# Kernel optimization log

Hardware: AMD Instinct MI355X
Metric: run time of the kernel (lower is better)

## Reference

```python
import jax, jax.numpy as jnp
import numpy as np

H = 8  # num_heads
NEG = -1000000.0

def _ln(x, g, b):
    m = jnp.mean(x, axis=-1, keepdims=True)
    v = jnp.var(x, axis=-1, keepdims=True)
    return (x - m) / jnp.sqrt(v + 1e-5) * g + b


def setup_inputs() -> dict:
    key = jax.random.key(0)
    ks = jax.random.split(key, 24)
    B, T, D = 8, 1024, 1024
    Lt, Nt, K, Rt, E = 768, 77, 2, 512, 2048
    s = 0.02
    r = lambda i, shape: s * jax.random.normal(ks[i], shape, jnp.float32)
    return {
        "x": jax.random.normal(ks[0], (B, T, D), jnp.float32),
        "xf": jax.random.normal(ks[1], (B, Nt, Lt), jnp.float32),
        "emb": jax.random.normal(ks[2], (B, E), jnp.float32),
        "src_mask": jnp.ones((B, T, 1), jnp.float32),
        "cond_type": jax.random.randint(ks[3], (B, 1, 1), 0, 100),
        "re_motion": jax.random.normal(ks[4], (B, K, Rt, D), jnp.float32),
        "re_text": jax.random.normal(ks[5], (B, K, 1, D), jnp.float32),
        "re_mask": jnp.ones((B, K, Rt), jnp.float32),
        "ln_g": jnp.ones((D,)), "ln_b": jnp.zeros((D,)),
        "tln_g": jnp.ones((Lt,)), "tln_b": jnp.zeros((Lt,)),
        "rn1_g": jnp.ones((2 * D,)), "rn1_b": jnp.zeros((2 * D,)),
        "rn2_g": jnp.ones((D,)), "rn2_b": jnp.zeros((D,)),
        "Wq": r(6, (D, D)), "bq": jnp.zeros((D,)),
        "Wkt": r(7, (Lt, D)), "bkt": jnp.zeros((D,)),
        "Wvt": r(8, (Lt, D)), "bvt": jnp.zeros((D,)),
        "Wkm": r(9, (D, D)), "bkm": jnp.zeros((D,)),
        "Wvm": r(10, (D, D)), "bvm": jnp.zeros((D,)),
        "Wkr": r(11, (2 * D, D)), "bkr": jnp.zeros((D,)),
        "Wvr": r(12, (D, D)), "bvr": jnp.zeros((D,)),  # zero-init in original; random here for nontrivial math
        "We": r(13, (E, 2 * D)), "be": jnp.zeros((2 * D,)),
        "sln_g": jnp.ones((D,)), "sln_b": jnp.zeros((D,)),
        "Wo": r(14, (D, D)), "bo": jnp.zeros((D,)),  # zero-init in original
    }


def reference(x, xf, emb, src_mask, cond_type, re_motion, re_text, re_mask,
              ln_g, ln_b, tln_g, tln_b, rn1_g, rn1_b, rn2_g, rn2_b,
              Wq, bq, Wkt, bkt, Wvt, bvt, Wkm, bkm, Wvm, bvm,
              Wkr, bkr, Wvr, bvr, We, be, sln_g, sln_b, Wo, bo):
    B, T, D = x.shape
    K, Rt = re_motion.shape[1], re_motion.shape[2]

    norm_x = _ln(x, ln_g, ln_b)
    norm_xf = _ln(xf, tln_g, tln_b)
    query = norm_x @ Wq + bq  # (B,T,D)

    text_ct = (cond_type % 10 > 0).astype(x.dtype)   # (B,1,1)
    retr_ct = (cond_type // 10 > 0).astype(x.dtype)  # (B,1,1)
    re_mask_r = re_mask.reshape(B, -1, 1)            # (B,K*Rt,1)

    # retrieval key features: concat(motion, repeated text) along channels
    re_text_rep = jnp.broadcast_to(re_text, (B, K, Rt, D))
    re_feat_key = jnp.concatenate([re_motion, re_text_rep], axis=-1).reshape(B, -1, 2 * D)

    key_text = norm_xf @ Wkt + bkt + (1.0 - text_ct) * NEG
    key_retr = _ln(re_feat_key, rn1_g, rn1_b) @ Wkr + bkr \
        + (1.0 - retr_ct) * NEG + (1.0 - re_mask_r) * NEG
    key_motion = norm_x @ Wkm + bkm + (1.0 - src_mask) * NEG
    key = jnp.concatenate([key_text, key_retr, key_motion], axis=1)  # (B,N,D)
    N = key.shape[1]

    q = jax.nn.softmax(query.reshape(B, T, H, -1), axis=-1)  # softmax over head dim
    k = jax.nn.softmax(key.reshape(B, N, H, -1), axis=1)     # softmax over tokens

    value_text = (norm_xf @ Wvt + bvt) * text_ct
    value_retr = (_ln(re_motion.reshape(B, -1, D), rn2_g, rn2_b) @ Wvr + bvr) * retr_ct * re_mask_r
    value_motion = (norm_x @ Wvm + bvm) * src_mask
    v = jnp.concatenate([value_text, value_retr, value_motion], axis=1).reshape(B, N, H, -1)

    att = jnp.einsum('bnhd,bnhl->bhdl', k, v)          # (B,H,dh,dh)
    y = jnp.einsum('bthd,bhdl->bthl', q, att).reshape(B, T, D)

    # StylizationBlock: FiLM from time embedding, then zero-init out proj (eval: dropout = id)
    eo = jax.nn.silu(emb) @ We + be                    # (B,2D)
    scale, shift = jnp.split(eo[:, None, :], 2, axis=2)
    h = _ln(y, sln_g, sln_b) * (1.0 + scale) + shift
    h = jax.nn.silu(h) @ Wo + bo
    return x + h
```

## Files before the change

### kernel.cpp

```cpp
#include <hip/hip_runtime.h>
#include <hip/hip_bf16.h>
#include <math.h>

using bf16 = __hip_bfloat16;

typedef short s16x8 __attribute__((ext_vector_type(8)));
typedef short s16x4 __attribute__((ext_vector_type(4)));
typedef float f32x4 __attribute__((ext_vector_type(4)));

constexpr int Bc = 8, Tc = 1024, Dc = 1024, Hc = 8;
constexpr int NTc = 77, LTc = 768, KRc = 1024, Nc = 2125, Ec = 2048;
constexpr float NEGC = -1000000.0f;

constexpr int NP = 2128;
constexpr long SKT = (long)Dc * NP;

constexpr long F_STATS1 = 0;
constexpr long F_STATS2 = F_STATS1 + 16384;
constexpr long F_KEYADD = F_STATS2 + 16384;
constexpr long F_VALMUL = F_KEYADD + 17000;
constexpr long F_SILU   = F_VALMUL + 17000;
constexpr long F_EO     = F_SILU + 16384;
constexpr long F_ATT    = F_EO + 16384;
constexpr long F_END    = F_ATT + 1048576;
// ... 158 lines not shown
__global__ __launch_bounds__(256) void transpose_all(
    const float* __restrict__ Wq,  const float* __restrict__ Wkt,
    const float* __restrict__ Wvt, const float* __restrict__ Wkm,
    const float* __restrict__ Wvm, const float* __restrict__ Wkr,
    const float* __restrict__ Wvr, const float* __restrict__ Wo,
    short* __restrict__ WtQ,  short* __restrict__ WtKT,
    short* __restrict__ WtVT, short* __restrict__ WtKM,
    short* __restrict__ WtVM, short* __restrict__ WtKR,
    short* __restrict__ WtVR, short* __restrict__ WtO) {
    __shared__ float t[32][33];
    int sy = blockIdx.y;
    const float* W; short* Wt; int K; int ky;
    if (sy < 32)       { W = Wq;  Wt = WtQ;  K = 1024; ky = sy; }
    else if (sy < 56)  { W = Wkt; Wt = WtKT; K = 768;  ky = sy - 32; }
    else if (sy < 80)  { W = Wvt; Wt = WtVT; K = 768;  ky = sy - 56; }
    else if (sy < 112) { W = Wkm; Wt = WtKM; K = 1024; ky = sy - 80; }
    else if (sy < 144) { W = Wvm; Wt = WtVM; K = 1024; ky = sy - 112; }
    else if (sy < 208) { W = Wkr; Wt = WtKR; K = 2048; ky = sy - 144; }
    else if (sy < 240) { W = Wvr; Wt = WtVR; K = 1024; ky = sy - 208; }
    else               { W = Wo;  Wt = WtO;  K = 1024; ky = sy - 240; }
    int n0 = blockIdx.x * 32, k0 = ky * 32;
    int tx = threadIdx.x & 31, ty = threadIdx.x >> 5;
    #pragma unroll
    for (int i = 0; i < 4; ++i)
        t[ty + i * 8][tx] = W[(long)(k0 + ty + i * 8) * 1024 + n0 + tx];
    __syncthreads();
    #pragma unroll
    for (int i = 0; i < 4; ++i)
        Wt[(long)(n0 + ty + i * 8) * K + k0 + tx] = f2s(t[tx][ty + i * 8]);
}

constexpr int LDK = 64;

template <typename TC, bool TR = false>
__global__ __launch_bounds__(256) void gemm_bt(
    const short* __restrict__ A, int lda, long sA,
    const short* __restrict__ Bt, int ldb,
    const float* __restrict__ bias,
    const float* __restrict__ rowadd, int sRA,
    const float* __restrict__ rowmul, int sRM,
    const float* __restrict__ addC, int ldac, long sAC,
    TC* __restrict__ C, int ldc, long sC,
    int M, int K) {
    int bz = blockIdx.z;
    A += (long)bz * sA;
    C += (long)bz * sC;
    if (rowadd) rowadd += (long)bz * sRA;
    if (rowmul) rowmul += (long)bz * sRM;
    if (addC) addC += (long)bz * sAC;

    const int tm = blockIdx.y * 128;
    const int tn = blockIdx.x * 128;

    __shared__ __align__(16) short As[128 * LDK];
    __shared__ __align__(16) short Bs[128 * LDK];

    int tid = threadIdx.x;
    int lane = tid & 63, wid = tid >> 6;
    int wi = wid >> 1, wj = wid & 1;
    int l16 = lane & 15, quad = lane >> 4;

    f32x4 acc[4][4];
    #pragma unroll
    for (int i = 0; i < 4; ++i)
        #pragma unroll
        for (int j = 0; j < 4; ++j)
            acc[i][j] = (f32x4){0.f, 0.f, 0.f, 0.f};

    auto issue = [&](int k0) {
        #pragma unroll
        for (int p = 0; p < 4; ++p) {
            int e = p * 256 + tid;
            int row = e >> 3, c8 = e & 7;
            int gm = tm + row;
            if (gm >= M) gm = M - 1;
            gl_lds16(A + (long)gm * lda + k0 + c8 * 8, &As[row * LDK + c8 * 8]);
            gl_lds16(Bt + (long)(tn + row) * ldb + k0 + c8 * 8, &Bs[row * LDK + c8 * 8]);
        }
    };

    issue(0);
    int kt = 0;
    while (true) {
        __syncthreads();
        #pragma unroll
        for (int kk = 0; kk < 2; ++kk) {
            s16x8 af[4], bfr[4];
            #pragma unroll
            for (int i = 0; i < 4; ++i)
                af[i] = *(const s16x8*)&As[(wi * 64 + i * 16 + l16) * LDK + kk * 32 + quad * 8];
            #pragma unroll
            for (int j = 0; j < 4; ++j)
                bfr[j] = *(const s16x8*)&Bs[(wj * 64 + j * 16 + l16) * LDK + kk * 32 + quad * 8];
            #pragma unroll
            for (int i = 0; i < 4; ++i)
                #pragma unroll
                for (int j = 0; j < 4; ++j) {
                    if constexpr (TR)
                        acc[i][j] = __builtin_amdgcn_mfma_f32_16x16x32_bf16(bfr[j], af[i], acc[i][j], 0, 0, 0);
                    else
                        acc[i][j] = __builtin_amdgcn_mfma_f32_16x16x32_bf16(af[i], bfr[j], acc[i][j], 0, 0, 0);
                }
        }
        int nxt = kt + 64;
        if (nxt >= K) break;
        __syncthreads();
        issue(nxt);
        kt = nxt;
    }

    if constexpr (TR) {
        #pragma unroll
        for (int j = 0; j < 4; ++j) {
            #pragma unroll
            for (int r = 0; r < 4; ++r) {
                int feat = tn + wj * 64 + j * 16 + quad * 4 + r;
                float bf_ = bias ? bias[feat] : 0.f;
                #pragma unroll
                for (int i = 0; i < 4; ++i) {
                    int tok = tm + wi * 64 + i * 16 + l16;
                    if (tok >= M) continue;
                    float v = acc[i][j][r] + bf_ + (rowadd ? rowadd[tok] : 0.f);
                    v *= (rowmul ? rowmul[tok] : 1.f);
                    storef(&C[(long)feat * ldc + tok], v);
                }
            }
        }
    } else {
        #pragma unroll
        for (int i = 0; i < 4; ++i) {
            #pragma unroll
            for (int r = 0; r < 4; ++r) {
                int gm = tm + wi * 64 + i * 16 + quad * 4 + r;
                if (gm >= M) continue;
                float ra = rowadd ? rowadd[gm] : 0.f;
                float rm = rowmul ? rowmul[gm] : 1.f;
                #pragma unroll
                for (int j = 0; j < 4; ++j) {
                    int gn = tn + wj * 64 + j * 16 + l16;
                    float v = acc[i][j][r] + (bias ? bias[gn] : 0.f) + ra;
                    v *= rm;
                    if (addC) v += addC[(long)gm * ldac + gn];
                    storef(&C[(long)gm * ldc + gn], v);
                }
            }
        }
    }
}

__global__ __launch_bounds__(256) void gemm_qkvm(
    const short* __restrict__ A, const short* __restrict__ Bt,
    const float* __restrict__ bq, const float* __restrict__ bkm,
    const float* __restrict__ bvm,
    const float* __restrict__ key_add, const float* __restrict__ val_mul,
    bf16* __restrict__ q16, bf16* __restrict__ kT, bf16* __restrict__ vT) {
    const int tm = blockIdx.y * 128;
    const int tn = blockIdx.x * 128;
    const int sec = tn >> 10;
    const int fn0 = tn & 1023;

    __shared__ __align__(16) short As[128 * LDK];
    __shared__ __align__(16) short Bs[128 * LDK];

    int tid = threadIdx.x;
    int lane = tid & 63, wid = tid >> 6;
    int wi = wid >> 1, wj = wid & 1;
    int l16 = lane & 15, quad = lane >> 4;

    f32x4 acc[4][4];
    #pragma unroll
    for (int i = 0; i < 4; ++i)
        #pragma unroll
        for (int j = 0; j < 4; ++j)
            acc[i][j] = (f32x4){0.f, 0.f, 0.f, 0.f};

    auto issue = [&](int k0) {
        #pragma unroll
        for (int p = 0; p < 4; ++p) {
            int e = p * 256 + tid;
            int row = e >> 3, c8 = e & 7;
            gl_lds16(A + (long)(tm + row) * 1024 + k0 + c8 * 8, &As[row * LDK + c8 * 8]);
            gl_lds16(Bt + (long)(tn + row) * 1024 + k0 + c8 * 8, &Bs[row * LDK + c8 * 8]);
        }
    };

    issue(0);
    int kt = 0;
    while (true) {
        __syncthreads();
        #pragma unroll
        for (int kk = 0; kk < 2; ++kk) {
            s16x8 af[4], bfr[4];
            #pragma unroll
            for (int i = 0; i < 4; ++i)
                af[i] = *(const s16x8*)&As[(wi * 64 + i * 16 + l16) * LDK + kk * 32 + quad * 8];
            #pragma unroll
            for (int j = 0; j < 4; ++j)
                bfr[j] = *(const s16x8*)&Bs[(wj * 64 + j * 16 + l16) * LDK + kk * 32 + quad * 8];
            if (sec == 0) {
                #pragma unroll
                for (int i = 0; i < 4; ++i)
                    #pragma unroll
                    for (int j = 0; j < 4; ++j)
                        acc[i][j] = __builtin_amdgcn_mfma_f32_16x16x32_bf16(af[i], bfr[j], acc[i][j], 0, 0, 0);
            } else {
                #pragma unroll
                for (int i = 0; i < 4; ++i)
                    #pragma unroll
                    for (int j = 0; j < 4; ++j)
                        acc[i][j] = __builtin_amdgcn_mfma_f32_16x16x32_bf16(bfr[j], af[i], acc[i][j], 0, 0, 0);
            }
        }
        int nxt = kt + 64;
        if (nxt >= 1024) break;
        __syncthreads();
        issue(nxt);
        kt = nxt;
    }

    if (sec == 0) {
        #pragma unroll
        for (int i = 0; i < 4; ++i) {
            #pragma unroll
            for (int r = 0; r < 4; ++r) {
                int gm = tm + wi * 64 + i * 16 + quad * 4 + r;
                #pragma unroll
                for (int j = 0; j < 4; ++j) {
                    int gn = fn0 + wj * 64 + j * 16 + l16;
                    q16[(long)gm * Dc + gn] = f2b(acc[i][j][r] + bq[gn]);
                }
            }
        }
    } else {
        const float* bias = (sec == 1) ? bkm : bvm;
        bf16* C = (sec == 1) ? kT : vT;
        #pragma unroll
        for (int j = 0; j < 4; ++j) {
            #pragma unroll
            for (int r = 0; r < 4; ++r) {
                int feat = fn0 + wj * 64 + j * 16 + quad * 4 + r;
                float bf_ = bias[feat];
                #pragma unroll
                for (int i = 0; i < 4; ++i) {
                    int gm = tm + wi * 64 + i * 16 + l16;
                    int b = gm >> 10, tok = gm & 1023;
                    int mi = b * Nc + NTc + KRc + tok;
                    float v = acc[i][j][r] + bf_;
                    if (sec == 1) v += key_add[mi];
                    else          v *= val_mul[mi];
                    C[(long)b * SKT + (long)feat * NP + NTc + KRc + tok] = f2b(v);
                }
            }
        }
    }
}

__global__ __launch_bounds__(256) void gemm_retr(
    const short* __restrict__ ren1, const short* __restrict__ ren2,
    const short* __restrict__ WtKR, const short* __restrict__ WtVR,
    const float* __restrict__ bkr, const float* __restrict__ bvr,
    const float* __restrict__ key_add, const float* __restrict__ val_mul,
    bf16* __restrict__ kT, bf16* __restrict__ vT) {
    int z = blockIdx.z;
    bool isK = z < 8;
    int b = isK ? z : z - 8;
    const short* A  = isK ? ren1 + (long)b * KRc * 2048 : ren2 + (long)b * KRc * 1024;
    const short* Bt = isK ? WtKR : WtVR;
    int K = isK ? 2048 : 1024;
    const float* bias = isK ? bkr : bvr;
    const float* rmask = (isK ? key_add : val_mul) + b * Nc + NTc;
    bf16* C = (isK ? kT : vT) + (long)b * SKT + NTc;

    const int tm = blockIdx.y * 128;
    const int tn = blockIdx.x * 128;

    __shared__ __align__(16) short As[128 * LDK];
    __shared__ __align__(16) short Bs[128 * LDK];

    int tid = threadIdx.x;
    int lane = tid & 63, wid = tid >> 6;
    int wi = wid >> 1, wj = wid & 1;
    int l16 = lane & 15, quad = lane >> 4;

    f32x4 acc[4][4];
    #pragma unroll
    for (int i = 0; i < 4; ++i)
        #pragma unroll
        for (int j = 0; j < 4; ++j)
            acc[i][j] = (f32x4){0.f, 0.f, 0.f, 0.f};

    auto issue = [&](int k0) {
        #pragma unroll
        for (int p = 0; p < 4; ++p) {
            int e = p * 256 + tid;
            int row = e >> 3, c8 = e & 7;
            gl_lds16(A + (long)(tm + row) * K + k0 + c8 * 8, &As[row * LDK + c8 * 8]);
            gl_lds16(Bt + (long)(tn + row) * K + k0 + c8 * 8, &Bs[row * LDK + c8 * 8]);
        }
    };

    issue(0);
    int kt = 0;
    while (true) {
        __syncthreads();
        #pragma unroll
        for (int kk = 0; kk < 2; ++kk) {
            s16x8 af[4], bfr[4];
            #pragma unroll
            for (int i = 0; i < 4; ++i)
                af[i] = *(const s16x8*)&As[(wi * 64 + i * 16 + l16) * LDK + kk * 32 + quad * 8];
            #pragma unroll
            for (int j = 0; j < 4; ++j)
                bfr[j] = *(const s16x8*)&Bs[(wj * 64 + j * 16 + l16) * LDK + kk * 32 + quad * 8];
            #pragma unroll
            for (int i = 0; i < 4; ++i)
                #pragma unroll
                for (int j = 0; j < 4; ++j)
                    acc[i][j] = __builtin_amdgcn_mfma_f32_16x16x32_bf16(bfr[j], af[i], acc[i][j], 0, 0, 0);
        }
        int nxt = kt + 64;
        if (nxt >= K) break;
        __syncthreads();
        issue(nxt);
        kt = nxt;
    }

    #pragma unroll
    for (int j = 0; j < 4; ++j) {
        #pragma unroll
        for (int r = 0; r < 4; ++r) {
            int feat = tn + wj * 64 + j * 16 + quad * 4 + r;
            float bf_ = bias[feat];
            #pragma unroll
            for (int i = 0; i < 4; ++i) {
                int tok = tm + wi * 64 + i * 16 + l16;
                float v = acc[i][j][r] + bf_;
                if (isK) v += rmask[tok];
                else     v *= rmask[tok];
                C[(long)feat * NP + tok] = f2b(v);
            }
        }
    }
}

__global__ __launch_bounds__(256) void eo_partial(const float* __restrict__ emb,
                                                  const float* __restrict__ We,
                                                  float* __restrict__ part) {
    int nb = blockIdx.x;
    int ks = blockIdx.y;
    int n = nb * 256 + threadIdx.x;
    int k0 = ks * 64;
    __shared__ float a_s[8][64];
    for (int idx = threadIdx.x; idx < 512; idx += 256) {
        int b = idx >> 6, kk = idx & 63;
        float v = emb[b * 2048 + k0 + kk];
        a_s[b][kk] = v / (1.f + expf(-v));
    }
    __syncthreads();
    float acc[8] = {};
    for (int kk = 0; kk < 64; ++kk) {
        float w = We[(long)(k0 + kk) * 2048 + n];
        #pragma unroll
        for (int b = 0; b < 8; ++b) acc[b] = fmaf(a_s[b][kk], w, acc[b]);
    }
    #pragma unroll
    for (int b = 0; b < 8; ++b) part[((long)ks * 8 + b) * 2048 + n] = acc[b];
}

__global__ __launch_bounds__(256) void eo_reduce(const float* __restrict__ part,
                                                 const float* __restrict__ be,
                                                 float* __restrict__ eo) {
    int idx = blockIdx.x * 256 + threadIdx.x;
// ... 310 lines not shown
    const float* bo  = (const float*)d_in[35];

    float* ws = (float*)d_ws;
    float* stats1   = ws + F_STATS1;
    float* stats2   = ws + F_STATS2;
    float* key_add  = ws + F_KEYADD;
    float* val_mul  = ws + F_VALMUL;
    float* cs_m     = ws + F_SILU;
    float* cs_inv   = cs_m + Bc * Dc;
    float* eo       = ws + F_EO;
    bf16*  attT     = (bf16*)(ws + F_ATT);
    bf16* wb = (bf16*)(ws + F_END);
    bf16* norm_x16 = wb + B_NORMX;
    bf16* q16      = wb + B_Q;
    bf16* kT16     = wb + B_KT;
    bf16* vT16     = wb + B_VT;
    bf16* nxf16    = wb + B_NXF;
    short* WtQ  = (short*)(wb + B_WQ);
    short* WtKM = (short*)(wb + B_WKM);
    short* WtVM = (short*)(wb + B_WVM);
    short* WtKT = (short*)(wb + B_WKT);
    short* WtVT = (short*)(wb + B_WVT);
    short* WtKR = (short*)(wb + B_WKR);
    short* WtVR = (short*)(wb + B_WVR);
    short* WtO  = (short*)(wb + B_WO);
    float* att_part = (float*)(wb + B_NORMX);
    bf16* y16 = wb + B_NORMX;
    bf16* s16 = q16;
    float* eo_part = (float*)(wb + B_VT);
    bf16* ren1 = (bf16*)d_out;
    bf16* ren2 = q16;

    float* out = (float*)d_out;
    const long sKT = SKT;

    ln_rows<bf16><<<dim3(Bc * Tc), dim3(256), 0, stream>>>(x, ln_g, ln_b, norm_x16, Dc);
    ln_rows<bf16><<<dim3(Bc * NTc), dim3(256), 0, stream>>>(xf, tln_g, tln_b, nxf16, LTc);
    ln_stats_both<<<dim3(Bc * KRc), dim3(256), 0, stream>>>(re_motion, re_text, stats1, stats2);

    prep_masks<<<dim3((Bc * Nc + 255) / 256), dim3(256), 0, stream>>>(
        cond_type, src_mask, re_mask, key_add, val_mul);
    zero_tail<<<dim3((Bc * Dc + 255) / 256), dim3(256), 0, stream>>>(vT16);

    transpose_all<<<dim3(32, 272), dim3(256), 0, stream>>>(
        Wq, Wkt, Wvt, Wkm, Wvm, Wkr, Wvr, Wo,
        WtQ, WtKT, WtVT, WtKM, WtVM, WtKR, WtVR, WtO);

    materialize_ren<<<dim3(Bc * KRc), dim3(256), 0, stream>>>(
        re_motion, re_text, stats1, stats2, rn1_g, rn1_b, rn2_g, rn2_b, ren1, ren2);

    gemm_bt<bf16, true><<<dim3(8, 1, Bc), dim3(256), 0, stream>>>(
        (const short*)nxf16, LTc, (long)NTc * LTc, WtKT, 768, bkt,
        key_add + 0, Nc, nullptr, 0, nullptr, 0, 0,
        kT16 + 0, NP, sKT, NTc, 768);
    gemm_bt<bf16, true><<<dim3(8, 1, Bc), dim3(256), 0, stream>>>(
        (const short*)nxf16, LTc, (long)NTc * LTc, WtVT, 768, bvt,
        nullptr, 0, val_mul + 0, Nc, nullptr, 0, 0,
        vT16 + 0, NP, sKT, NTc, 768);

    gemm_retr<<<dim3(8, 8, 16), dim3(256), 0, stream>>>(
        (const short*)ren1, (const short*)ren2, WtKR, WtVR, bkr, bvr,
        key_add, val_mul, kT16, vT16);

    gemm_qkvm<<<dim3(24, 64), dim3(256), 0, stream>>>(
        (const short*)norm_x16, WtQ, bq, bkm, bvm, key_add, val_mul,
        q16, kT16, vT16);

    softmax_head<<<dim3(Bc * Tc * Hc / 4), dim3(256), 0, stream>>>(q16);
    ksm_rows<<<dim3(Bc * Dc / 4), dim3(256), 0, stream>>>(kT16, cs_m, cs_inv);

    att_gemm<<<dim3(Bc * Hc, ATT_SPLIT), dim3(256), 0, stream>>>(kT16, vT16, cs_m, att_part);
    reduce_att_t<<<dim3((64 * 16384 + 255) / 256), dim3(256), 0, stream>>>(att_part, cs_inv, attT);

    y_gemm<<<dim3(Tc / 128, Bc * Hc), dim3(256), 0, stream>>>(q16, attT, y16);

    eo_partial<<<dim3(8, 32), dim3(256), 0, stream>>>(emb, We, eo_part);
    eo_reduce<<<dim3(64), dim3(256), 0, stream>>>(eo_part, be, eo);

    film_kernel<<<dim3(Bc * Tc), dim3(256), 0, stream>>>(y16, eo, sln_g, sln_b, s16);

    gemm_bt<float, false><<<dim3(8, 64, 1), dim3(256), 0, stream>>>(
        (const short*)s16, Dc, 0, WtO, 1024, bo, nullptr, 0, nullptr, 0,
        x, Dc, 0, out, Dc, 0, Bc * Tc, 1024);
}
```

Measured before the change: 695.3 us.

## Use 256x256 double-buffered GEMM tiles and fuse text key/value projections

The 128x128 single-buffered GEMM kernels (q/k/v motion, retrieval, output projection) become 256x256-tile, 512-thread kernels. Each has two LDS buffers so the next K-slice loads while MFMAs run on the current one. The two separate text key/value GEMM launches merge into one kernel that picks weights and masks by column section. The goal is more data reuse per LDS load, hidden global-load latency and one fewer launch, at the cost of about 128KB of LDS per block and far fewer blocks, e.g. 128 for the output GEMM and 384 for qkvm. That leaves CUs idle or creates uneven waves.

```diff
diff --git a/kernel.cpp b/kernel.cpp
--- a/kernel.cpp
+++ b/kernel.cpp
@@ -214,25 +214,17 @@
 
 constexpr int LDK = 64;
 
-template <typename TC, bool TR = false>
-__global__ __launch_bounds__(256) void gemm_bt(
-    const short* __restrict__ A, int lda, long sA,
-    const short* __restrict__ Bt, int ldb,
-    const float* __restrict__ bias,
-    const float* __restrict__ rowadd, int sRA,
-    const float* __restrict__ rowmul, int sRM,
-    const float* __restrict__ addC, int ldac, long sAC,
-    TC* __restrict__ C, int ldc, long sC,
-    int M, int K) {
-    int bz = blockIdx.z;
-    A += (long)bz * sA;
-    C += (long)bz * sC;
-    if (rowadd) rowadd += (long)bz * sRA;
-    if (rowmul) rowmul += (long)bz * sRM;
-    if (addC) addC += (long)bz * sAC;
-
-    const int tm = blockIdx.y * 128;
+__global__ __launch_bounds__(256) void gemm_text(
+    const short* __restrict__ A,
+    const short* __restrict__ Bt,
+    const float* __restrict__ bkt, const float* __restrict__ bvt,
+    const float* __restrict__ key_add, const float* __restrict__ val_mul,
+    bf16* __restrict__ kT, bf16* __restrict__ vT) {
+    int b = blockIdx.z;
+    A += (long)b * NTc * LTc;
     const int tn = blockIdx.x * 128;
+    const int sec = tn >> 10;
+    const int fn0 = tn & 1023;
 
     __shared__ __align__(16) short As[128 * LDK];
     __shared__ __align__(16) short Bs[128 * LDK];
@@ -254,10 +246,10 @@
         for (int p = 0; p < 4; ++p) {
             int e = p * 256 + tid;
             int row = e >> 3, c8 = e & 7;
-            int gm = tm + row;
-            if (gm >= M) gm = M - 1;
-            gl_lds16(A + (long)gm * lda + k0 + c8 * 8, &As[row * LDK + c8 * 8]);
-            gl_lds16(Bt + (long)(tn + row) * ldb + k0 + c8 * 8, &Bs[row * LDK + c8 * 8]);
+            int gm = row;
+            if (gm >= NTc) gm = NTc - 1;
+            gl_lds16(A + (long)gm * LTc + k0 + c8 * 8, &As[row * LDK + c8 * 8]);
+            gl_lds16(Bt + (long)(tn + row) * LTc + k0 + c8 * 8, &Bs[row * LDK + c8 * 8]);
         }
     };
 
@@ -277,138 +269,208 @@
             #pragma unroll
             for (int i = 0; i < 4; ++i)
                 #pragma unroll
-                for (int j = 0; j < 4; ++j) {
-                    if constexpr (TR)
-                        acc[i][j] = __builtin_amdgcn_mfma_f32_16x16x32_bf16(bfr[j], af[i], acc[i][j], 0, 0, 0);
-                    else
-                        acc[i][j] = __builtin_amdgcn_mfma_f32_16x16x32_bf16(af[i], bfr[j], acc[i][j], 0, 0, 0);
-                }
+                for (int j = 0; j < 4; ++j)
+                    acc[i][j] = __builtin_amdgcn_mfma_f32_16x16x32_bf16(bfr[j], af[i], acc[i][j], 0, 0, 0);
         }
         int nxt = kt + 64;
-        if (nxt >= K) break;
+        if (nxt >= 768) break;
         __syncthreads();
         issue(nxt);
         kt = nxt;
     }
 
-    if constexpr (TR) {
-        #pragma unroll
-        for (int j = 0; j < 4; ++j) {
-            #pragma unroll
-            for (int r = 0; r < 4; ++r) {
-                int feat = tn + wj * 64 + j * 16 + quad * 4 + r;
-                float bf_ = bias ? bias[feat] : 0.f;
+    const float* bias = sec ? bvt : bkt;
+    const float* rmask = (sec ? val_mul : key_add) + b * Nc;
+    bf16* C = (sec ? vT : kT) + (long)b * SKT;
+    #pragma unroll
+    for (int j = 0; j < 4; ++j) {
+        #pragma unroll
+        for (int r = 0; r < 4; ++r) {
+            int feat = fn0 + wj * 64 + j * 16 + quad * 4 + r;
+            float bf_ = bias[feat];
+            #pragma unroll
+            for (int i = 0; i < 4; ++i) {
+                int tok = wi * 64 + i * 16 + l16;
+                if (tok >= NTc) continue;
+                float v = acc[i][j][r] + bf_;
+                if (sec) v *= rmask[tok];
+                else     v += rmask[tok];
+                C[(long)feat * NP + tok] = f2b(v);
+            }
+        }
+    }
+}
+
+constexpr int BK2 = 64;
+
+template <typename TC>
+__global__ __launch_bounds__(512, 2) void gemm_bt2(
+    const short* __restrict__ A, int lda,
+    const short* __restrict__ Bt, int ldb,
+    const float* __restrict__ bias,
+    const float* __restrict__ addC, int ldac,
+    TC* __restrict__ C, int ldc, int K) {
+    const int tm = blockIdx.y * 256;
+    const int tn = blockIdx.x * 256;
+
+    __shared__ __align__(16) short As[2][256 * BK2];
+    __shared__ __align__(16) short Bs[2][256 * BK2];
+
+    int tid = threadIdx.x;
+    int lane = tid & 63, wid = tid >> 6;
+    int wr = wid >> 2, wc = wid & 3;
+    int l16 = lane & 15, quad = lane >> 4;
+
+    f32x4 acc[8][4];
+    #pragma unroll
+    for (int i = 0; i < 8; ++i)
+        #pragma unroll
+        for (int j = 0; j < 4; ++j)
+            acc[i][j] = (f32x4){0.f, 0.f, 0.f, 0.f};
+
+    auto stage = [&](int k0, int buf) {
+        #pragma unroll
+        for (int p = 0; p < 4; ++p) {
+            int e = p * 512 + tid;
+            int row = e >> 3, c8 = (e & 7) * 8;
+            gl_lds16(A + (long)(tm + row) * lda + k0 + c8, &As[buf][row * BK2 + c8]);
+            gl_lds16(Bt + (long)(tn + row) * ldb + k0 + c8, &Bs[buf][row * BK2 + c8]);
+        }
+    };
+    auto compute = [&](int buf) {
+        const short* as = As[buf];
+        const short* bs = Bs[buf];
+        #pragma unroll
+        for (int kk = 0; kk < 2; ++kk) {
+            s16x8 af[8], bfr[4];
+            #pragma unroll
+            for (int i = 0; i < 8; ++i)
+                af[i] = *(const s16x8*)&as[(wr * 128 + i * 16 + l16) * BK2 + kk * 32 + quad * 8];
+            #pragma unroll
+            for (int j = 0; j < 4; ++j)
+                bfr[j] = *(const s16x8*)&bs[(wc * 64 + j * 16 + l16) * BK2 + kk * 32 + quad * 8];
+            #pragma unroll
+            for (int i = 0; i < 8; ++i)
                 #pragma unroll
-                for (int i = 0; i < 4; ++i) {
-                    int tok = tm + wi * 64 + i * 16 + l16;
-                    if (tok >= M) continue;
-                    float v = acc[i][j][r] + bf_ + (rowadd ? rowadd[tok] : 0.f);
-                    v *= (rowmul ? rowmul[tok] : 1.f);
-                    storef(&C[(long)feat * ldc + tok], v);
-                }
+                for (int j = 0; j < 4; ++j)
+                    acc[i][j] = __builtin_amdgcn_mfma_f32_16x16x32_bf16(af[i], bfr[j], acc[i][j], 0, 0, 0);
+        }
+    };
+
+    stage(0, 0);
+    __syncthreads();
+    int cur = 0, kt = 0;
+    while (true) {
+        int nxt = kt + BK2;
+        if (nxt < K) stage(nxt, cur ^ 1);
+        compute(cur);
+        if (nxt >= K) break;
+        __syncthreads();
+        cur ^= 1;
+        kt = nxt;
+    }
+
+    #pragma unroll
+    for (int i = 0; i < 8; ++i) {
+        #pragma unroll
+        for (int r = 0; r < 4; ++r) {
+            int gm = tm + wr * 128 + i * 16 + quad * 4 + r;
+            #pragma unroll
+            for (int j = 0; j < 4; ++j) {
+                int gn = tn + wc * 64 + j * 16 + l16;
+                float v = acc[i][j][r] + bias[gn];
+                if (addC) v += addC[(long)gm * ldac + gn];
+                storef(&C[(long)gm * ldc + gn], v);
             }
         }
-    } else {
-        #pragma unroll
-        for (int i = 0; i < 4; ++i) {
-            #pragma unroll
-            for (int r = 0; r < 4; ++r) {
-                int gm = tm + wi * 64 + i * 16 + quad * 4 + r;
-                if (gm >= M) continue;
-                float ra = rowadd ? rowadd[gm] : 0.f;
-                float rm = rowmul ? rowmul[gm] : 1.f;
-                #pragma unroll
-                for (int j = 0; j < 4; ++j) {
-                    int gn = tn + wj * 64 + j * 16 + l16;
-                    float v = acc[i][j][r] + (bias ? bias[gn] : 0.f) + ra;
-                    v *= rm;
-                    if (addC) v += addC[(long)gm * ldac + gn];
-                    storef(&C[(long)gm * ldc + gn], v);
-                }
-            }
-        }
-    }
-}
-
-__global__ __launch_bounds__(256) void gemm_qkvm(
+    }
+}
+
+__global__ __launch_bounds__(512, 2) void gemm_qkvm2(
     const short* __restrict__ A, const short* __restrict__ Bt,
     const float* __restrict__ bq, const float* __restrict__ bkm,
     const float* __restrict__ bvm,
     const float* __restrict__ key_add, const float* __restrict__ val_mul,
     bf16* __restrict__ q16, bf16* __restrict__ kT, bf16* __restrict__ vT) {
-    const int tm = blockIdx.y * 128;
-    const int tn = blockIdx.x * 128;
+    const int tm = blockIdx.y * 256;
+    const int tn = blockIdx.x * 256;
     const int sec = tn >> 10;
     const int fn0 = tn & 1023;
 
-    __shared__ __align__(16) short As[128 * LDK];
-    __shared__ __align__(16) short Bs[128 * LDK];
+    __shared__ __align__(16) short As[2][256 * BK2];
+    __shared__ __align__(16) short Bs[2][256 * BK2];
 
     int tid = threadIdx.x;
     int lane = tid & 63, wid = tid >> 6;
-    int wi = wid >> 1, wj = wid & 1;
+    int wr = wid >> 2, wc = wid & 3;
     int l16 = lane & 15, quad = lane >> 4;
 
-    f32x4 acc[4][4];
-    #pragma unroll
-    for (int i = 0; i < 4; ++i)
+    f32x4 acc[8][4];
+    #pragma unroll
+    for (int i = 0; i < 8; ++i)
         #pragma unroll
         for (int j = 0; j < 4; ++j)
             acc[i][j] = (f32x4){0.f, 0.f, 0.f, 0.f};
 
-    auto issue = [&](int k0) {
+    auto stage = [&](int k0, int buf) {
         #pragma unroll
         for (int p = 0; p < 4; ++p) {
-            int e = p * 256 + tid;
-            int row = e >> 3, c8 = e & 7;
-            gl_lds16(A + (long)(tm + row) * 1024 + k0 + c8 * 8, &As[row * LDK + c8 * 8]);
-            gl_lds16(Bt + (long)(tn + row) * 1024 + k0 + c8 * 8, &Bs[row * LDK + c8 * 8]);
+            int e = p * 512 + tid;
+            int row = e >> 3, c8 = (e & 7) * 8;
+            gl_lds16(A + (long)(tm + row) * 1024 + k0 + c8, &As[buf][row * BK2 + c8]);
+            gl_lds16(Bt + (long)(tn + row) * 1024 + k0 + c8, &Bs[buf][row * BK2 + c8]);
         }
     };
-
-    issue(0);
-    int kt = 0;
-    while (true) {
-        __syncthreads();
+    auto compute = [&](int buf) {
+        const short* as = As[buf];
+        const short* bs = Bs[buf];
         #pragma unroll
         for (int kk = 0; kk < 2; ++kk) {
-            s16x8 af[4], bfr[4];
-            #pragma unroll
-            for (int i = 0; i < 4; ++i)
-                af[i] = *(const s16x8*)&As[(wi * 64 + i * 16 + l16) * LDK + kk * 32 + quad * 8];
+            s16x8 af[8], bfr[4];
+            #pragma unroll
+            for (int i = 0; i < 8; ++i)
+                af[i] = *(const s16x8*)&as[(wr * 128 + i * 16 + l16) * BK2 + kk * 32 + quad * 8];
             #pragma unroll
             for (int j = 0; j < 4; ++j)
-                bfr[j] = *(const s16x8*)&Bs[(wj * 64 + j * 16 + l16) * LDK + kk * 32 + quad * 8];
+                bfr[j] = *(const s16x8*)&bs[(wc * 64 + j * 16 + l16) * BK2 + kk * 32 + quad * 8];
             if (sec == 0) {
                 #pragma unroll
-                for (int i = 0; i < 4; ++i)
+                for (int i = 0; i < 8; ++i)
                     #pragma unroll
                     for (int j = 0; j < 4; ++j)
                         acc[i][j] = __builtin_amdgcn_mfma_f32_16x16x32_bf16(af[i], bfr[j], acc[i][j], 0, 0, 0);
             } else {
                 #pragma unroll
-                for (int i = 0; i < 4; ++i)
+                for (int i = 0; i < 8; ++i)
                     #pragma unroll
                     for (int j = 0; j < 4; ++j)
                         acc[i][j] = __builtin_amdgcn_mfma_f32_16x16x32_bf16(bfr[j], af[i], acc[i][j], 0, 0, 0);
             }
         }
-        int nxt = kt + 64;
+    };
+
+    stage(0, 0);
+    __syncthreads();
+    int cur = 0, kt = 0;
+    while (true) {
+        int nxt = kt + BK2;
+        if (nxt < 1024) stage(nxt, cur ^ 1);
+        compute(cur);
         if (nxt >= 1024) break;
         __syncthreads();
-        issue(nxt);
+        cur ^= 1;
         kt = nxt;
     }
 
     if (sec == 0) {
         #pragma unroll
-        for (int i = 0; i < 4; ++i) {
+        for (int i = 0; i < 8; ++i) {
             #pragma unroll
             for (int r = 0; r < 4; ++r) {
-                int gm = tm + wi * 64 + i * 16 + quad * 4 + r;
+                int gm = tm + wr * 128 + i * 16 + quad * 4 + r;
                 #pragma unroll
                 for (int j = 0; j < 4; ++j) {
-                    int gn = fn0 + wj * 64 + j * 16 + l16;
+                    int gn = fn0 + wc * 64 + j * 16 + l16;
                     q16[(long)gm * Dc + gn] = f2b(acc[i][j][r] + bq[gn]);
                 }
             }
@@ -420,11 +482,11 @@
         for (int j = 0; j < 4; ++j) {
             #pragma unroll
             for (int r = 0; r < 4; ++r) {
-                int feat = fn0 + wj * 64 + j * 16 + quad * 4 + r;
+                int feat = fn0 + wc * 64 + j * 16 + quad * 4 + r;
                 float bf_ = bias[feat];
                 #pragma unroll
-                for (int i = 0; i < 4; ++i) {
-                    int gm = tm + wi * 64 + i * 16 + l16;
+                for (int i = 0; i < 8; ++i) {
+                    int gm = tm + wr * 128 + i * 16 + l16;
                     int b = gm >> 10, tok = gm & 1023;
                     int mi = b * Nc + NTc + KRc + tok;
                     float v = acc[i][j][r] + bf_;
@@ -437,7 +499,7 @@
     }
 }
 
-__global__ __launch_bounds__(256) void gemm_retr(
+__global__ __launch_bounds__(512, 2) void gemm_retr2(
     const short* __restrict__ ren1, const short* __restrict__ ren2,
     const short* __restrict__ WtKR, const short* __restrict__ WtVR,
     const float* __restrict__ bkr, const float* __restrict__ bvr,
@@ -453,57 +515,63 @@
     const float* rmask = (isK ? key_add : val_mul) + b * Nc + NTc;
     bf16* C = (isK ? kT : vT) + (long)b * SKT + NTc;
 
-    const int tm = blockIdx.y * 128;
-    const int tn = blockIdx.x * 128;
-
-    __shared__ __align__(16) short As[128 * LDK];
-    __shared__ __align__(16) short Bs[128 * LDK];
+    const int tm = blockIdx.y * 256;
+    const int tn = blockIdx.x * 256;
+
+    __shared__ __align__(16) short As[2][256 * BK2];
+    __shared__ __align__(16) short Bs[2][256 * BK2];
 
     int tid = threadIdx.x;
     int lane = tid & 63, wid = tid >> 6;
-    int wi = wid >> 1, wj = wid & 1;
+    int wr = wid >> 2, wc = wid & 3;
     int l16 = lane & 15, quad = lane >> 4;
 
-    f32x4 acc[4][4];
-    #pragma unroll
-    for (int i = 0; i < 4; ++i)
+    f32x4 acc[8][4];
+    #pragma unroll
+    for (int i = 0; i < 8; ++i)
         #pragma unroll
         for (int j = 0; j < 4; ++j)
             acc[i][j] = (f32x4){0.f, 0.f, 0.f, 0.f};
 
-    auto issue = [&](int k0) {
+    auto stage = [&](int k0, int buf) {
         #pragma unroll
         for (int p = 0; p < 4; ++p) {
-            int e = p * 256 + tid;
-            int row = e >> 3, c8 = e & 7;
-            gl_lds16(A + (long)(tm + row) * K + k0 + c8 * 8, &As[row * LDK + c8 * 8]);
-            gl_lds16(Bt + (long)(tn + row) * K + k0 + c8 * 8, &Bs[row * LDK + c8 * 8]);
+            int e = p * 512 + tid;
+            int row = e >> 3, c8 = (e & 7) * 8;
+            gl_lds16(A + (long)(tm + row) * K + k0 + c8, &As[buf][row * BK2 + c8]);
+            gl_lds16(Bt + (long)(tn + row) * K + k0 + c8, &Bs[buf][row * BK2 + c8]);
         }
     };
-
-    issue(0);
-    int kt = 0;
-    while (true) {
-        __syncthreads();
+    auto compute = [&](int buf) {
+        const short* as = As[buf];
+        const short* bs = Bs[buf];
         #pragma unroll
         for (int kk = 0; kk < 2; ++kk) {
-            s16x8 af[4], bfr[4];
-            #pragma unroll
-            for (int i = 0; i < 4; ++i)
-                af[i] = *(const s16x8*)&As[(wi * 64 + i * 16 + l16) * LDK + kk * 32 + quad * 8];
+            s16x8 af[8], bfr[4];
+            #pragma unroll
+            for (int i = 0; i < 8; ++i)
+                af[i] = *(const s16x8*)&as[(wr * 128 + i * 16 + l16) * BK2 + kk * 32 + quad * 8];
             #pragma unroll
             for (int j = 0; j < 4; ++j)
-                bfr[j] = *(const s16x8*)&Bs[(wj * 64 + j * 16 + l16) * LDK + kk * 32 + quad * 8];
-            #pragma unroll
-            for (int i = 0; i < 4; ++i)
+                bfr[j] = *(const s16x8*)&bs[(wc * 64 + j * 16 + l16) * BK2 + kk * 32 + quad * 8];
+            #pragma unroll
+            for (int i = 0; i < 8; ++i)
                 #pragma unroll
                 for (int j = 0; j < 4; ++j)
                     acc[i][j] = __builtin_amdgcn_mfma_f32_16x16x32_bf16(bfr[j], af[i], acc[i][j], 0, 0, 0);
         }
-        int nxt = kt + 64;
+    };
+
+    stage(0, 0);
+    __syncthreads();
+    int cur = 0, kt = 0;
+    while (true) {
+        int nxt = kt + BK2;
+        if (nxt < K) stage(nxt, cur ^ 1);
+        compute(cur);
         if (nxt >= K) break;
         __syncthreads();
-        issue(nxt);
+        cur ^= 1;
         kt = nxt;
     }
 
@@ -511,11 +579,11 @@
     for (int j = 0; j < 4; ++j) {
         #pragma unroll
         for (int r = 0; r < 4; ++r) {
-            int feat = tn + wj * 64 + j * 16 + quad * 4 + r;
+            int feat = tn + wc * 64 + j * 16 + quad * 4 + r;
             float bf_ = bias[feat];
             #pragma unroll
-            for (int i = 0; i < 4; ++i) {
-                int tok = tm + wi * 64 + i * 16 + l16;
+            for (int i = 0; i < 8; ++i) {
+                int tok = tm + wr * 128 + i * 16 + l16;
                 float v = acc[i][j][r] + bf_;
                 if (isK) v += rmask[tok];
                 else     v *= rmask[tok];
@@ -896,7 +964,6 @@
     bf16* ren2 = q16;
 
     float* out = (float*)d_out;
-    const long sKT = SKT;
 
     ln_rows<bf16><<<dim3(Bc * Tc), dim3(256), 0, stream>>>(x, ln_g, ln_b, norm_x16, Dc);
     ln_rows<bf16><<<dim3(Bc * NTc), dim3(256), 0, stream>>>(xf, tln_g, tln_b, nxf16, LTc);
@@ -913,20 +980,14 @@
     materialize_ren<<<dim3(Bc * KRc), dim3(256), 0, stream>>>(
         re_motion, re_text, stats1, stats2, rn1_g, rn1_b, rn2_g, rn2_b, ren1, ren2);
 
-    gemm_bt<bf16, true><<<dim3(8, 1, Bc), dim3(256), 0, stream>>>(
-        (const short*)nxf16, LTc, (long)NTc * LTc, WtKT, 768, bkt,
-        key_add + 0, Nc, nullptr, 0, nullptr, 0, 0,
-        kT16 + 0, NP, sKT, NTc, 768);
-    gemm_bt<bf16, true><<<dim3(8, 1, Bc), dim3(256), 0, stream>>>(
-        (const short*)nxf16, LTc, (long)NTc * LTc, WtVT, 768, bvt,
-        nullptr, 0, val_mul + 0, Nc, nullptr, 0, 0,
-        vT16 + 0, NP, sKT, NTc, 768);
-
-    gemm_retr<<<dim3(8, 8, 16), dim3(256), 0, stream>>>(
+    gemm_text<<<dim3(16, 1, Bc), dim3(256), 0, stream>>>(
+        (const short*)nxf16, WtKT, bkt, bvt, key_add, val_mul, kT16, vT16);
+
+    gemm_retr2<<<dim3(4, 4, 16), dim3(512), 0, stream>>>(
         (const short*)ren1, (const short*)ren2, WtKR, WtVR, bkr, bvr,
         key_add, val_mul, kT16, vT16);
 
-    gemm_qkvm<<<dim3(24, 64), dim3(256), 0, stream>>>(
+    gemm_qkvm2<<<dim3(12, 32), dim3(512), 0, stream>>>(
         (const short*)norm_x16, WtQ, bq, bkm, bvm, key_add, val_mul,
         q16, kT16, vT16);
 
@@ -943,7 +1004,6 @@
 
     film_kernel<<<dim3(Bc * Tc), dim3(256), 0, stream>>>(y16, eo, sln_g, sln_b, s16);
 
-    gemm_bt<float, false><<<dim3(8, 64, 1), dim3(256), 0, stream>>>(
-        (const short*)s16, Dc, 0, WtO, 1024, bo, nullptr, 0, nullptr, 0,
-        x, Dc, 0, out, Dc, 0, Bc * Tc, 1024);
-}
+    gemm_bt2<float><<<dim3(4, 32), dim3(512), 0, stream>>>(
+        (const short*)s16, 1024, WtO, 1024, bo, x, 1024, out, 1024, 1024);
+}
```

Result: slower. 1.038 ms (+49.2%).

## Merge projection GEMMs into one launch with XCD-aware tile swizzling

Applied to the files above, without the earlier changes.

Folds the retrieval-key, Q/Km/Vm and text K/V projection GEMMs into a single flat-grid kernel. Each block picks its section, operand pointers, MFMA operand order and epilogue from its block index. The retrieval-value GEMM is split into its own kernel, and the output-projection GEMM gets the same block-index swizzle. The swizzle groups tiles that share operands by the 8-way XCD round-robin, aiming to improve L2 reuse. The goal is to cut launch overhead and tail underfill from many small launches. The risks are extra branching in the merged kernel and an assumption that the text key and value transposed weights are contiguous.

```diff
diff --git a/kernel.cpp b/kernel.cpp
--- a/kernel.cpp
+++ b/kernel.cpp
@@ -214,25 +214,42 @@
 
 constexpr int LDK = 64;
 
-template <typename TC, bool TR = false>
-__global__ __launch_bounds__(256) void gemm_bt(
-    const short* __restrict__ A, int lda, long sA,
-    const short* __restrict__ Bt, int ldb,
-    const float* __restrict__ bias,
-    const float* __restrict__ rowadd, int sRA,
-    const float* __restrict__ rowmul, int sRM,
-    const float* __restrict__ addC, int ldac, long sAC,
-    TC* __restrict__ C, int ldc, long sC,
-    int M, int K) {
-    int bz = blockIdx.z;
-    A += (long)bz * sA;
-    C += (long)bz * sC;
-    if (rowadd) rowadd += (long)bz * sRA;
-    if (rowmul) rowmul += (long)bz * sRM;
-    if (addC) addC += (long)bz * sAC;
-
-    const int tm = blockIdx.y * 128;
-    const int tn = blockIdx.x * 128;
+__global__ __launch_bounds__(256) void gemm_mega(
+    const short* __restrict__ norm_x, const short* __restrict__ ren1,
+    const short* __restrict__ nxf,
+    const short* __restrict__ WtQKVM, const short* __restrict__ WtKR,
+    const short* __restrict__ WtTXT,
+    const float* __restrict__ bq, const float* __restrict__ bkm,
+    const float* __restrict__ bvm, const float* __restrict__ bkr,
+    const float* __restrict__ bkt, const float* __restrict__ bvt,
+    const float* __restrict__ key_add, const float* __restrict__ val_mul,
+    bf16* __restrict__ q16, bf16* __restrict__ kT, bf16* __restrict__ vT) {
+    int jid = blockIdx.x;
+    int sect, tm, tn, K, M, lda, bb = 0;
+    const short* A; const short* Bt;
+    if (jid < 512) {
+        sect = 0;
+        int s = (jid & 7) * 64 + (jid >> 3);
+        bb = s >> 6; int r = s & 63;
+        tm = (r >> 3) * 128; tn = (r & 7) * 128;
+        A = ren1 + (long)bb * KRc * 2048; lda = 2048; K = 2048; M = 1024;
+        Bt = WtKR;
+    } else if (jid < 2048) {
+        sect = 1;
+        int l = jid - 512;
+        int s = (l & 7) * 192 + (l >> 3);
+        tn = (s % 24) * 128; tm = (s / 24) * 128;
+        A = norm_x; lda = 1024; K = 1024; M = 8192;
+        Bt = WtQKVM;
+    } else {
+        sect = 2;
+        int l = jid - 2048;
+        bb = l >> 4; tn = (l & 15) * 128; tm = 0;
+        A = nxf + (long)bb * NTc * LTc; lda = 768; K = 768; M = 77;
+        Bt = WtTXT;
+    }
+    const int ldb = lda;
+    const bool swap_ops = !(sect == 1 && tn < 1024);
 
     __shared__ __align__(16) short As[128 * LDK];
     __shared__ __align__(16) short Bs[128 * LDK];
@@ -274,15 +291,19 @@
             #pragma unroll
             for (int j = 0; j < 4; ++j)
                 bfr[j] = *(const s16x8*)&Bs[(wj * 64 + j * 16 + l16) * LDK + kk * 32 + quad * 8];
-            #pragma unroll
-            for (int i = 0; i < 4; ++i)
+            if (swap_ops) {
                 #pragma unroll
-                for (int j = 0; j < 4; ++j) {
-                    if constexpr (TR)
+                for (int i = 0; i < 4; ++i)
+                    #pragma unroll
+                    for (int j = 0; j < 4; ++j)
                         acc[i][j] = __builtin_amdgcn_mfma_f32_16x16x32_bf16(bfr[j], af[i], acc[i][j], 0, 0, 0);
-                    else
+            } else {
+                #pragma unroll
+                for (int i = 0; i < 4; ++i)
+                    #pragma unroll
+                    for (int j = 0; j < 4; ++j)
                         acc[i][j] = __builtin_amdgcn_mfma_f32_16x16x32_bf16(af[i], bfr[j], acc[i][j], 0, 0, 0);
-                }
+            }
         }
         int nxt = kt + 64;
         if (nxt >= K) break;
@@ -291,116 +312,7 @@
         kt = nxt;
     }
 
-    if constexpr (TR) {
-        #pragma unroll
-        for (int j = 0; j < 4; ++j) {
-            #pragma unroll
-            for (int r = 0; r < 4; ++r) {
-                int feat = tn + wj * 64 + j * 16 + quad * 4 + r;
-                float bf_ = bias ? bias[feat] : 0.f;
-                #pragma unroll
-                for (int i = 0; i < 4; ++i) {
-                    int tok = tm + wi * 64 + i * 16 + l16;
-                    if (tok >= M) continue;
-                    float v = acc[i][j][r] + bf_ + (rowadd ? rowadd[tok] : 0.f);
-                    v *= (rowmul ? rowmul[tok] : 1.f);
-                    storef(&C[(long)feat * ldc + tok], v);
-                }
-            }
-        }
-    } else {
-        #pragma unroll
-        for (int i = 0; i < 4; ++i) {
-            #pragma unroll
-            for (int r = 0; r < 4; ++r) {
-                int gm = tm + wi * 64 + i * 16 + quad * 4 + r;
-                if (gm >= M) continue;
-                float ra = rowadd ? rowadd[gm] : 0.f;
-                float rm = rowmul ? rowmul[gm] : 1.f;
-                #pragma unroll
-                for (int j = 0; j < 4; ++j) {
-                    int gn = tn + wj * 64 + j * 16 + l16;
-                    float v = acc[i][j][r] + (bias ? bias[gn] : 0.f) + ra;
-                    v *= rm;
-                    if (addC) v += addC[(long)gm * ldac + gn];
-                    storef(&C[(long)gm * ldc + gn], v);
-                }
-            }
-        }
-    }
-}
-
-__global__ __launch_bounds__(256) void gemm_qkvm(
-    const short* __restrict__ A, const short* __restrict__ Bt,
-    const float* __restrict__ bq, const float* __restrict__ bkm,
-    const float* __restrict__ bvm,
-    const float* __restrict__ key_add, const float* __restrict__ val_mul,
-    bf16* __restrict__ q16, bf16* __restrict__ kT, bf16* __restrict__ vT) {
-    const int tm = blockIdx.y * 128;
-    const int tn = blockIdx.x * 128;
-    const int sec = tn >> 10;
-    const int fn0 = tn & 1023;
-
-    __shared__ __align__(16) short As[128 * LDK];
-    __shared__ __align__(16) short Bs[128 * LDK];
-
-    int tid = threadIdx.x;
-    int lane = tid & 63, wid = tid >> 6;
-    int wi = wid >> 1, wj = wid & 1;
-    int l16 = lane & 15, quad = lane >> 4;
-
-    f32x4 acc[4][4];
-    #pragma unroll
-    for (int i = 0; i < 4; ++i)
-        #pragma unroll
-        for (int j = 0; j < 4; ++j)
-            acc[i][j] = (f32x4){0.f, 0.f, 0.f, 0.f};
-
-    auto issue = [&](int k0) {
-        #pragma unroll
-        for (int p = 0; p < 4; ++p) {
-            int e = p * 256 + tid;
-            int row = e >> 3, c8 = e & 7;
-            gl_lds16(A + (long)(tm + row) * 1024 + k0 + c8 * 8, &As[row * LDK + c8 * 8]);
-            gl_lds16(Bt + (long)(tn + row) * 1024 + k0 + c8 * 8, &Bs[row * LDK + c8 * 8]);
-        }
-    };
-
-    issue(0);
-    int kt = 0;
-    while (true) {
-        __syncthreads();
-        #pragma unroll
-        for (int kk = 0; kk < 2; ++kk) {
-            s16x8 af[4], bfr[4];
-            #pragma unroll
-            for (int i = 0; i < 4; ++i)
-                af[i] = *(const s16x8*)&As[(wi * 64 + i * 16 + l16) * LDK + kk * 32 + quad * 8];
-            #pragma unroll
-            for (int j = 0; j < 4; ++j)
-                bfr[j] = *(const s16x8*)&Bs[(wj * 64 + j * 16 + l16) * LDK + kk * 32 + quad * 8];
-            if (sec == 0) {
-                #pragma unroll
-                for (int i = 0; i < 4; ++i)
-                    #pragma unroll
-                    for (int j = 0; j < 4; ++j)
-                        acc[i][j] = __builtin_amdgcn_mfma_f32_16x16x32_bf16(af[i], bfr[j], acc[i][j], 0, 0, 0);
-            } else {
-                #pragma unroll
-                for (int i = 0; i < 4; ++i)
-                    #pragma unroll
-                    for (int j = 0; j < 4; ++j)
-                        acc[i][j] = __builtin_amdgcn_mfma_f32_16x16x32_bf16(bfr[j], af[i], acc[i][j], 0, 0, 0);
-            }
-        }
-        int nxt = kt + 64;
-        if (nxt >= 1024) break;
-        __syncthreads();
-        issue(nxt);
-        kt = nxt;
-    }
-
-    if (sec == 0) {
+    if (sect == 1 && tn < 1024) {
         #pragma unroll
         for (int i = 0; i < 4; ++i) {
             #pragma unroll
@@ -408,12 +320,13 @@
                 int gm = tm + wi * 64 + i * 16 + quad * 4 + r;
                 #pragma unroll
                 for (int j = 0; j < 4; ++j) {
-                    int gn = fn0 + wj * 64 + j * 16 + l16;
+                    int gn = tn + wj * 64 + j * 16 + l16;
                     q16[(long)gm * Dc + gn] = f2b(acc[i][j][r] + bq[gn]);
                 }
             }
         }
-    } else {
+    } else if (sect == 1) {
+        int sec = tn >> 10, fn0 = tn & 1023;
         const float* bias = (sec == 1) ? bkm : bvm;
         bf16* C = (sec == 1) ? kT : vT;
         #pragma unroll
@@ -434,27 +347,58 @@
                 }
             }
         }
-    }
-}
-
-__global__ __launch_bounds__(256) void gemm_retr(
-    const short* __restrict__ ren1, const short* __restrict__ ren2,
-    const short* __restrict__ WtKR, const short* __restrict__ WtVR,
-    const float* __restrict__ bkr, const float* __restrict__ bvr,
-    const float* __restrict__ key_add, const float* __restrict__ val_mul,
-    bf16* __restrict__ kT, bf16* __restrict__ vT) {
-    int z = blockIdx.z;
-    bool isK = z < 8;
-    int b = isK ? z : z - 8;
-    const short* A  = isK ? ren1 + (long)b * KRc * 2048 : ren2 + (long)b * KRc * 1024;
-    const short* Bt = isK ? WtKR : WtVR;
-    int K = isK ? 2048 : 1024;
-    const float* bias = isK ? bkr : bvr;
-    const float* rmask = (isK ? key_add : val_mul) + b * Nc + NTc;
-    bf16* C = (isK ? kT : vT) + (long)b * SKT + NTc;
-
-    const int tm = blockIdx.y * 128;
-    const int tn = blockIdx.x * 128;
+    } else if (sect == 0) {
+        const float* rmask = key_add + bb * Nc + NTc;
+        bf16* C = kT + (long)bb * SKT + NTc;
+        #pragma unroll
+        for (int j = 0; j < 4; ++j) {
+            #pragma unroll
+            for (int r = 0; r < 4; ++r) {
+                int feat = tn + wj * 64 + j * 16 + quad * 4 + r;
+                float bf_ = bkr[feat];
+                #pragma unroll
+                for (int i = 0; i < 4; ++i) {
+                    int tok = tm + wi * 64 + i * 16 + l16;
+                    C[(long)feat * NP + tok] = f2b(acc[i][j][r] + bf_ + rmask[tok]);
+                }
+            }
+        }
+    } else {
+        int sec = tn >> 10, fn0 = tn & 1023;
+        const float* bias = sec ? bvt : bkt;
+        const float* rmask = (sec ? val_mul : key_add) + bb * Nc;
+        bf16* C = (sec ? vT : kT) + (long)bb * SKT;
+        #pragma unroll
+        for (int j = 0; j < 4; ++j) {
+            #pragma unroll
+            for (int r = 0; r < 4; ++r) {
+                int feat = fn0 + wj * 64 + j * 16 + quad * 4 + r;
+                float bf_ = bias[feat];
+                #pragma unroll
+                for (int i = 0; i < 4; ++i) {
+                    int tok = wi * 64 + i * 16 + l16;
+                    if (tok >= NTc) continue;
+                    float v = acc[i][j][r] + bf_;
+                    if (sec) v *= rmask[tok];
+                    else     v += rmask[tok];
+                    C[(long)feat * NP + tok] = f2b(v);
+                }
+            }
+        }
+    }
+}
+
+__global__ __launch_bounds__(256) void gemm_vr(
+    const short* __restrict__ ren2, const short* __restrict__ WtVR,
+    const float* __restrict__ bvr, const float* __restrict__ val_mul,
+    bf16* __restrict__ vT) {
+    int s = (blockIdx.x & 7) * 64 + (blockIdx.x >> 3);
+    int b = s >> 6; int r = s & 63;
+    const int tm = (r >> 3) * 128;
+    const int tn = (r & 7) * 128;
+    const short* A = ren2 + (long)b * KRc * 1024;
+    const float* rmask = val_mul + b * Nc + NTc;
+    bf16* C = vT + (long)b * SKT + NTc;
 
     __shared__ __align__(16) short As[128 * LDK];
     __shared__ __align__(16) short Bs[128 * LDK];
@@ -476,8 +420,8 @@
         for (int p = 0; p < 4; ++p) {
             int e = p * 256 + tid;
             int row = e >> 3, c8 = e & 7;
-            gl_lds16(A + (long)(tm + row) * K + k0 + c8 * 8, &As[row * LDK + c8 * 8]);
-            gl_lds16(Bt + (long)(tn + row) * K + k0 + c8 * 8, &Bs[row * LDK + c8 * 8]);
+            gl_lds16(A + (long)(tm + row) * 1024 + k0 + c8 * 8, &As[row * LDK + c8 * 8]);
+            gl_lds16(WtVR + (long)(tn + row) * 1024 + k0 + c8 * 8, &Bs[row * LDK + c8 * 8]);
         }
     };
 
@@ -499,6 +443,91 @@
                 #pragma unroll
                 for (int j = 0; j < 4; ++j)
                     acc[i][j] = __builtin_amdgcn_mfma_f32_16x16x32_bf16(bfr[j], af[i], acc[i][j], 0, 0, 0);
+        }
+        int nxt = kt + 64;
+        if (nxt >= 1024) break;
+        __syncthreads();
+        issue(nxt);
+        kt = nxt;
+    }
+
+    #pragma unroll
+    for (int j = 0; j < 4; ++j) {
+        #pragma unroll
+        for (int r2 = 0; r2 < 4; ++r2) {
+            int feat = tn + wj * 64 + j * 16 + quad * 4 + r2;
+            float bf_ = bvr[feat];
+            #pragma unroll
+            for (int i = 0; i < 4; ++i) {
+                int tok = tm + wi * 64 + i * 16 + l16;
+                C[(long)feat * NP + tok] = f2b((acc[i][j][r2] + bf_) * rmask[tok]);
+            }
+        }
+    }
+}
+
+template <typename TC>
+__global__ __launch_bounds__(256) void gemm_bt(
+    const short* __restrict__ A, int lda,
+    const short* __restrict__ Bt, int ldb,
+    const float* __restrict__ bias,
+    const float* __restrict__ addC, int ldac,
+    TC* __restrict__ C, int ldc, int K) {
+    int nx = gridDim.x;
+    int nwg = nx * gridDim.y;
+    int lin = blockIdx.y * nx + blockIdx.x;
+    int bx = blockIdx.x, by = blockIdx.y;
+    if ((nwg & 7) == 0) {
+        int chunk = nwg >> 3;
+        int swz = (lin & 7) * chunk + (lin >> 3);
+        bx = swz % nx; by = swz / nx;
+    }
+    const int tm = by * 128;
+    const int tn = bx * 128;
+
+    __shared__ __align__(16) short As[128 * LDK];
+    __shared__ __align__(16) short Bs[128 * LDK];
+
+    int tid = threadIdx.x;
+    int lane = tid & 63, wid = tid >> 6;
+    int wi = wid >> 1, wj = wid & 1;
+    int l16 = lane & 15, quad = lane >> 4;
+
+    f32x4 acc[4][4];
+    #pragma unroll
+    for (int i = 0; i < 4; ++i)
+        #pragma unroll
+        for (int j = 0; j < 4; ++j)
+            acc[i][j] = (f32x4){0.f, 0.f, 0.f, 0.f};
+
+    auto issue = [&](int k0) {
+        #pragma unroll
+        for (int p = 0; p < 4; ++p) {
+            int e = p * 256 + tid;
+            int row = e >> 3, c8 = e & 7;
+            gl_lds16(A + (long)(tm + row) * lda + k0 + c8 * 8, &As[row * LDK + c8 * 8]);
+            gl_lds16(Bt + (long)(tn + row) * ldb + k0 + c8 * 8, &Bs[row * LDK + c8 * 8]);
+        }
+    };
+
+    issue(0);
+    int kt = 0;
+    while (true) {
+        __syncthreads();
+        #pragma unroll
+        for (int kk = 0; kk < 2; ++kk) {
+            s16x8 af[4], bfr[4];
+            #pragma unroll
+            for (int i = 0; i < 4; ++i)
+                af[i] = *(const s16x8*)&As[(wi * 64 + i * 16 + l16) * LDK + kk * 32 + quad * 8];
+            #pragma unroll
+            for (int j = 0; j < 4; ++j)
+                bfr[j] = *(const s16x8*)&Bs[(wj * 64 + j * 16 + l16) * LDK + kk * 32 + quad * 8];
+            #pragma unroll
+            for (int i = 0; i < 4; ++i)
+                #pragma unroll
+                for (int j = 0; j < 4; ++j)
+                    acc[i][j] = __builtin_amdgcn_mfma_f32_16x16x32_bf16(af[i], bfr[j], acc[i][j], 0, 0, 0);
         }
         int nxt = kt + 64;
         if (nxt >= K) break;
@@ -508,18 +537,16 @@
     }
 
     #pragma unroll
-    for (int j = 0; j < 4; ++j) {
+    for (int i = 0; i < 4; ++i) {
         #pragma unroll
         for (int r = 0; r < 4; ++r) {
-            int feat = tn + wj * 64 + j * 16 + quad * 4 + r;
-            float bf_ = bias[feat];
-            #pragma unroll
-            for (int i = 0; i < 4; ++i) {
-                int tok = tm + wi * 64 + i * 16 + l16;
-                float v = acc[i][j][r] + bf_;
-                if (isK) v += rmask[tok];
-                else     v *= rmask[tok];
-                C[(long)feat * NP + tok] = f2b(v);
+            int gm = tm + wi * 64 + i * 16 + quad * 4 + r;
+            #pragma unroll
+            for (int j = 0; j < 4; ++j) {
+                int gn = tn + wj * 64 + j * 16 + l16;
+                float v = acc[i][j][r] + bias[gn];
+                if (addC) v += addC[(long)gm * ldac + gn];
+                storef(&C[(long)gm * ldc + gn], v);
             }
         }
     }
@@ -896,7 +923,6 @@
     bf16* ren2 = q16;
 
     float* out = (float*)d_out;
-    const long sKT = SKT;
 
     ln_rows<bf16><<<dim3(Bc * Tc), dim3(256), 0, stream>>>(x, ln_g, ln_b, norm_x16, Dc);
     ln_rows<bf16><<<dim3(Bc * NTc), dim3(256), 0, stream>>>(xf, tln_g, tln_b, nxf16, LTc);
@@ -913,22 +939,14 @@
     materialize_ren<<<dim3(Bc * KRc), dim3(256), 0, stream>>>(
         re_motion, re_text, stats1, stats2, rn1_g, rn1_b, rn2_g, rn2_b, ren1, ren2);
 
-    gemm_bt<bf16, true><<<dim3(8, 1, Bc), dim3(256), 0, stream>>>(
-        (const short*)nxf16, LTc, (long)NTc * LTc, WtKT, 768, bkt,
-        key_add + 0, Nc, nullptr, 0, nullptr, 0, 0,
-        kT16 + 0, NP, sKT, NTc, 768);
-    gemm_bt<bf16, true><<<dim3(8, 1, Bc), dim3(256), 0, stream>>>(
-        (const short*)nxf16, LTc, (long)NTc * LTc, WtVT, 768, bvt,
-        nullptr, 0, val_mul + 0, Nc, nullptr, 0, 0,
-        vT16 + 0, NP, sKT, NTc, 768);
-
-    gemm_retr<<<dim3(8, 8, 16), dim3(256), 0, stream>>>(
-        (const short*)ren1, (const short*)ren2, WtKR, WtVR, bkr, bvr,
-        key_add, val_mul, kT16, vT16);
-
-    gemm_qkvm<<<dim3(24, 64), dim3(256), 0, stream>>>(
-        (const short*)norm_x16, WtQ, bq, bkm, bvm, key_add, val_mul,
-        q16, kT16, vT16);
+    gemm_vr<<<dim3(512), dim3(256), 0, stream>>>(
+        (const short*)ren2, WtVR, bvr, val_mul, vT16);
+
+    gemm_mega<<<dim3(2176), dim3(256), 0, stream>>>(
+        (const short*)norm_x16, (const short*)ren1, (const short*)nxf16,
+        WtQ, WtKR, WtKT,
+        bq, bkm, bvm, bkr, bkt, bvt,
+        key_add, val_mul, q16, kT16, vT16);
 
     softmax_head<<<dim3(Bc * Tc * Hc / 4), dim3(256), 0, stream>>>(q16);
     ksm_rows<<<dim3(Bc * Dc / 4), dim3(256), 0, stream>>>(kT16, cs_m, cs_inv);
@@ -943,7 +961,6 @@
 
     film_kernel<<<dim3(Bc * Tc), dim3(256), 0, stream>>>(y16, eo, sln_g, sln_b, s16);
 
-    gemm_bt<float, false><<<dim3(8, 64, 1), dim3(256), 0, stream>>>(
-        (const short*)s16, Dc, 0, WtO, 1024, bo, nullptr, 0, nullptr, 0,
-        x, Dc, 0, out, Dc, 0, Bc * Tc, 1024);
-}
+    gemm_bt<float><<<dim3(8, 64), dim3(256), 0, stream>>>(
+        (const short*)s16, 1024, WtO, 1024, bo, x, 1024, out, 1024, 1024);
+}
```

Result: faster. 636.8 us (-8.4%).
